# Optimization experiments

Hardware: AMD Instinct MI355X
Metric: run time of the kernel (lower is better)

Reference implementation:

```python
import jax, jax.numpy as jnp
import numpy as np

B, T, C = 512, 256, 384
HEAD = 64

def setup_inputs() -> dict:
    key = jax.random.key(0)
    k1, k2, k3, k4 = jax.random.split(key, 4)
    x = jax.random.normal(k1, (B, T, C), dtype=jnp.float32)
    Wq = jax.random.normal(k2, (C, HEAD), dtype=jnp.float32) * (C ** -0.5)
    Wk = jax.random.normal(k3, (C, HEAD), dtype=jnp.float32) * (C ** -0.5)
    Wv = jax.random.normal(k4, (C, HEAD), dtype=jnp.float32) * (C ** -0.5)
    return {"x": x, "Wq": Wq, "Wk": Wk, "Wv": Wv}

def reference(x, Wq, Wk, Wv):
    # projections (Linear with bias=False): x @ W
    q = jnp.einsum('btc,ch->bth', x, Wq)   # [B,T,H]
    k = jnp.einsum('btc,ch->bth', x, Wk)   # [B,T,H]
    v = jnp.einsum('btc,ch->bth', x, Wv)   # [B,T,H]
    Cdim = x.shape[-1]
    # NOTE: original scales by C**-0.5 where C = nEmbd (not headSize)
    scores = jnp.einsum('bth,bsh->bts', q, k) * (Cdim ** -0.5)  # [B,T,T]
    Tlen = x.shape[1]
    causal = jnp.tril(jnp.ones((Tlen, Tlen), dtype=bool))
    scores = jnp.where(causal, scores, -jnp.inf)
    wei = jax.nn.softmax(scores, axis=-1)
    # dropout omitted (eval mode / deterministic reference)
    out = jnp.einsum('bts,bsh->bth', wei, v)  # [B,T,H]
    return out
```

## Files before the change

kernel.cpp:

```cpp
#include <hip/hip_runtime.h>

#define B_ 512
#define T_ 256
#define C_ 384
#define H_ 64
#define WT_STRIDE (H_ * C_)

typedef __bf16 bf16;
typedef bf16  bf16x8 __attribute__((ext_vector_type(8)));
typedef float f32x4  __attribute__((ext_vector_type(4)));

__global__ void prep_wt(const float* __restrict__ Wq,
                        const float* __restrict__ Wk,
                        const float* __restrict__ Wv,
                        bf16* __restrict__ wt)
{
    int idx = blockIdx.x * 256 + threadIdx.x;
    if (idx >= 3 * WT_STRIDE) return;
    int mat = idx / WT_STRIDE;
    int r   = idx % WT_STRIDE;
    int h   = r / C_;
    int k   = r % C_;
    const float* W = (mat == 0) ? Wq : (mat == 1) ? Wk : Wv;
    wt[idx] = (bf16)W[k * H_ + h];
}

__device__ __forceinline__ bf16x8 cvt8(float4 a, float4 b)
{
    bf16x8 r;
    r[0] = (bf16)a.x; r[1] = (bf16)a.y; r[2] = (bf16)a.z; r[3] = (bf16)a.w;
    r[4] = (bf16)b.x; r[5] = (bf16)b.y; r[6] = (bf16)b.z; r[7] = (bf16)b.w;
    return r;
}

#define SWZ(row, col) ((col) ^ (((row) & 7) << 3))

__device__ __forceinline__ const bf16x8* wts_frag(const bf16* wt_s, int mc, int kk)
{
    int byte = ((mc * 192 + kk) * 2) ^ ((mc & 7) << 4);
    return reinterpret_cast<const bf16x8*>(reinterpret_cast<const char*>(wt_s) + byte);
}

template<int USE_WT>
__global__ __launch_bounds__(512, 1)
void head_fused5(const float* __restrict__ x,
                 const float* __restrict__ Wq,
                 const float* __restrict__ Wk,
                 const float* __restrict__ Wv,
                 const bf16* __restrict__ wt,
                 float* __restrict__ out)
{
    __shared__ bf16 wt_s[3 * 64 * 192];
    __shared__ bf16 k_s[T_ * 64];
    __shared__ bf16 vT_s[H_ * 256];
    __shared__ bf16 p_s[8 * 16 * 64];

    const int tid  = threadIdx.x;
    const int wave = tid >> 6;
    const int lane = tid & 63;
    const int lr   = lane & 15;
    const int lg   = lane >> 4;

    const int b = blockIdx.x;
    const float* xb = x + (size_t)b * T_ * C_;
    bf16* pw = &p_s[wave * 16 * 64];

    bf16x8 qf[2][2];

    #pragma unroll
    for (int p = 0; p < 2; ++p) {
        const int mt = p ? (15 - wave) : wave;
        f32x4 acc[3][4];
        #pragma unroll
        for (int a = 0; a < 3; ++a)
            #pragma unroll
            for (int nw = 0; nw < 4; ++nw)
                acc[a][nw] = (f32x4){0.f, 0.f, 0.f, 0.f};

        #pragma unroll
        for (int half = 0; half < 2; ++half) {
            __syncthreads();
            if (USE_WT) {
                bf16x8 v[9];
                #pragma unroll
                for (int c = 0; c < 9; ++c) {
                    int f16 = c * 512 + tid;
                    int mc  = f16 / 24;
                    int kkc = f16 % 24;
                    v[c] = *reinterpret_cast<const bf16x8*>(
                        wt + mc * 384 + half * 192 + kkc * 8);
                }
                #pragma unroll
                for (int c = 0; c < 9; ++c) {
                    int f16 = c * 512 + tid;
                    int mc  = f16 / 24;
                    int kkc = f16 % 24;
                    int byte = ((mc * 192 + kkc * 8) * 2) ^ ((mc & 7) << 4);
                    *reinterpret_cast<bf16x8*>(
                        reinterpret_cast<char*>(wt_s) + byte) = v[c];
                }
            } else {
                #pragma unroll
                for (int c = 0; c < 9; ++c) {
                    int f16 = c * 512 + tid;
                    int mc  = f16 / 24;
                    int kkc = f16 % 24;
                    int mat = mc >> 6, col = mc & 63;
                    const float* W = (mat == 0) ? Wq : (mat == 1) ? Wk : Wv;
                    bf16x8 vv;
                    #pragma unroll
                    for (int j = 0; j < 8; ++j)
                        vv[j] = (bf16)W[(half * 192 + kkc * 8 + j) * H_ + col];
                    int byte = ((mc * 192 + kkc * 8) * 2) ^ ((mc & 7) << 4);
                    *reinterpret_cast<bf16x8*>(
                        reinterpret_cast<char*>(wt_s) + byte) = vv;
                }
            }
            __syncthreads();

            const float* xrow = xb + (mt * 16 + lr) * C_ + half * 192 + lg * 8;
            float4 xa[6][2];
            #pragma unroll
            for (int ks = 0; ks < 6; ++ks) {
                xa[ks][0] = *reinterpret_cast<const float4*>(xrow + ks * 32);
                xa[ks][1] = *reinterpret_cast<const float4*>(xrow + ks * 32 + 4);
            }
            #pragma unroll
            for (int ks = 0; ks < 6; ++ks) {
                bf16x8 af = cvt8(xa[ks][0], xa[ks][1]);
                const int kk = ks * 32 + lg * 8;
                #pragma unroll
                for (int nw = 0; nw < 4; ++nw) {
                    const int col = nw * 16 + lr;
                    acc[0][nw] = __builtin_amdgcn_mfma_f32_16x16x32_bf16(
                        af, *wts_frag(wt_s, col, kk), acc[0][nw], 0, 0, 0);
                    acc[1][nw] = __builtin_amdgcn_mfma_f32_16x16x32_bf16(
                        af, *wts_frag(wt_s, 64 + col, kk), acc[1][nw], 0, 0, 0);
                    acc[2][nw] = __builtin_amdgcn_mfma_f32_16x16x32_bf16(
                        af, *wts_frag(wt_s, 128 + col, kk), acc[2][nw], 0, 0, 0);
                }
            }
        }

        #pragma unroll
        for (int nw = 0; nw < 4; ++nw) {
            #pragma unroll
            for (int r = 0; r < 4; ++r) {
                int row = mt * 16 + lg * 4 + r;
                int col = nw * 16 + lr;
                k_s[row * 64 + SWZ(row, col)]   = (bf16)acc[1][nw][r];
                vT_s[col * 256 + SWZ(col, row)] = (bf16)acc[2][nw][r];
            }
        }
        #pragma unroll
        for (int nw = 0; nw < 4; ++nw) {
            #pragma unroll
            for (int r = 0; r < 4; ++r) {
                int row = lg * 4 + r;
                pw[row * 64 + SWZ(row, nw * 16 + lr)] = (bf16)acc[0][nw][r];
            }
        }
        asm volatile("s_waitcnt lgkmcnt(0)" ::: "memory");
        __builtin_amdgcn_sched_barrier(0);
        qf[p][0] = *reinterpret_cast<const bf16x8*>(&pw[lr * 64 + SWZ(lr, lg * 8)]);
        qf[p][1] = *reinterpret_cast<const bf16x8*>(&pw[lr * 64 + SWZ(lr, 32 + lg * 8)]);
    }
    __syncthreads();

    const float scale = 0.051031036307982884f;

    #pragma unroll
    for (int p = 0; p < 2; ++p) {
        const int mt  = p ? (15 - wave) : wave;
        const int nkt = mt + 1;

        float m[4], l[4];
        f32x4 oacc[4];
        #pragma unroll
        for (int r = 0; r < 4; ++r) { m[r] = -1e30f; l[r] = 0.f; }
        #pragma unroll
        for (int n = 0; n < 4; ++n) oacc[n] = (f32x4){0.f, 0.f, 0.f, 0.f};

        #pragma unroll
        for (int h = 0; h < 2; ++h) {
            const int vh = (nkt - h * 8) < 8 ? (nkt - h * 8) : 8;
            if (vh > 0) {
                float s[8][4];
                #pragma unroll
                for (int j = 0; j < 8; ++j) {
                    const int kt = h * 8 + j;
                    if (j < vh) {
                        bf16x8 kf0 = *reinterpret_cast<const bf16x8*>(
                            &k_s[(kt * 16 + lr) * 64 + SWZ(lr, lg * 8)]);
                        bf16x8 kf1 = *reinterpret_cast<const bf16x8*>(
                            &k_s[(kt * 16 + lr) * 64 + SWZ(lr, 32 + lg * 8)]);
                        f32x4 sc = (f32x4){0.f, 0.f, 0.f, 0.f};
                        sc = __builtin_amdgcn_mfma_f32_16x16x32_bf16(qf[p][0], kf0, sc, 0, 0, 0);
                        sc = __builtin_amdgcn_mfma_f32_16x16x32_bf16(qf[p][1], kf1, sc, 0, 0, 0);
                        #pragma unroll
                        for (int r = 0; r < 4; ++r) {
                            float v = sc[r] * scale;
                            if (kt == mt && lr > lg * 4 + r) v = -1e30f;
                            s[j][r] = v;
                        }
                    } else {
                        #pragma unroll
                        for (int r = 0; r < 4; ++r) s[j][r] = -1e30f;
                    }
                }

                float f[4];
                #pragma unroll
                for (int r = 0; r < 4; ++r) {
                    float pm = s[0][r];
                    #pragma unroll
                    for (int j = 1; j < 8; ++j) pm = fmaxf(pm, s[j][r]);
                    pm = fmaxf(pm, __shfl_xor(pm, 1));
                    pm = fmaxf(pm, __shfl_xor(pm, 2));
                    pm = fmaxf(pm, __shfl_xor(pm, 4));
                    pm = fmaxf(pm, __shfl_xor(pm, 8));
                    float nm = fmaxf(m[r], pm);
                    f[r] = __expf(m[r] - nm);
                    m[r] = nm;
                    l[r] *= f[r];
                }
                #pragma unroll
                for (int n = 0; n < 4; ++n)
                    #pragma unroll
                    for (int r = 0; r < 4; ++r)
                        oacc[n][r] *= f[r];

                #pragma unroll
                for (int r = 0; r < 4; ++r) {
                    float t = 0.f;
                    #pragma unroll
                    for (int j = 0; j < 8; ++j) {
                        float e = __expf(s[j][r] - m[r]);
                        s[j][r] = e;
                        t += e;
                    }
                    t += __shfl_xor(t, 1);
                    t += __shfl_xor(t, 2);
                    t += __shfl_xor(t, 4);
                    t += __shfl_xor(t, 8);
                    l[r] += t;
                }

                const int nkk = (vh + 1) >> 1;
                #pragma unroll
                for (int kkl = 0; kkl < 4; ++kkl) {
                    if (kkl < nkk) {
                        const int kk = h * 4 + kkl;
                        #pragma unroll
                        for (int r = 0; r < 4; ++r) {
                            int row = lg * 4 + r;
                            pw[row * 64 + SWZ(row, lr)]      = (bf16)s[2 * kkl][r];
                            pw[row * 64 + SWZ(row, 16 + lr)] = (bf16)s[2 * kkl + 1][r];
                        }
                        asm volatile("s_waitcnt lgkmcnt(0)" ::: "memory");
                        __builtin_amdgcn_sched_barrier(0);
                        bf16x8 pf = *reinterpret_cast<const bf16x8*>(
                            &pw[lr * 64 + SWZ(lr, lg * 8)]);
                        #pragma unroll
                        for (int n = 0; n < 4; ++n) {
                            bf16x8 vf = *reinterpret_cast<const bf16x8*>(
                                &vT_s[(n * 16 + lr) * 256 + SWZ(lr, kk * 32 + lg * 8)]);
                            oacc[n] = __builtin_amdgcn_mfma_f32_16x16x32_bf16(pf, vf, oacc[n], 0, 0, 0);
                        }
                    }
                }
            }
        }

        float rin[4];
        #pragma unroll
        for (int r = 0; r < 4; ++r) rin[r] = 1.0f / l[r];
        float* op = out + ((size_t)b * T_ + mt * 16) * H_;
        #pragma unroll
        for (int n = 0; n < 4; ++n)
            #pragma unroll
            for (int r = 0; r < 4; ++r)
                op[(lg * 4 + r) * H_ + n * 16 + lr] = oacc[n][r] * rin[r];
    }
}

extern "C" void kernel_launch(void* const* d_in, const int* in_sizes, int n_in,
                              void* d_out, int out_size, void* d_ws, size_t ws_size,
                              hipStream_t stream)
{
    (void)in_sizes; (void)n_in; (void)out_size;
    const float* x  = (const float*)d_in[0];
    const float* Wq = (const float*)d_in[1];
    const float* Wk = (const float*)d_in[2];
    const float* Wv = (const float*)d_in[3];
    float* o = (float*)d_out;

    if (ws_size >= (size_t)(3 * WT_STRIDE * sizeof(bf16))) {
        bf16* wt = (bf16*)d_ws;
        prep_wt<<<dim3((3 * WT_STRIDE + 255) / 256), dim3(256), 0, stream>>>(Wq, Wk, Wv, wt);
        head_fused5<1><<<dim3(B_), dim3(512), 0, stream>>>(x, Wq, Wk, Wv, wt, o);
    } else {
        head_fused5<0><<<dim3(B_), dim3(512), 0, stream>>>(x, Wq, Wk, Wv, nullptr, o);
    }
}
```

Baseline: 76.99 us.

## Process both query tiles per weight stage and prefetch all x fragments upfront

The QKV projection loop is restructured so each wave handles both of its row tiles in a single pass over each weight half. Weights are staged into shared memory twice instead of four times, and each weight fragment read from LDS feeds two MFMAs. All x rows for both tiles and both halves are loaded and converted to bf16 before any compute, so global loads are issued early. The cost is much higher register pressure (48 bf16x8 A fragments plus 24 accumulators), which could cause spills at 512 threads per block.

New measurement: 94.50 us. 22.7% more time.

```diff
diff --git a/kernel.cpp b/kernel.cpp
--- a/kernel.cpp
+++ b/kernel.cpp
@@ -43,7 +43,7 @@
 
 template<int USE_WT>
 __global__ __launch_bounds__(512, 1)
-void head_fused5(const float* __restrict__ x,
+void head_fused6(const float* __restrict__ x,
                  const float* __restrict__ Wq,
                  const float* __restrict__ Wk,
                  const float* __restrict__ Wv,
@@ -66,90 +66,102 @@
     bf16* pw = &p_s[wave * 16 * 64];
 
     bf16x8 qf[2][2];
-
-    #pragma unroll
-    for (int p = 0; p < 2; ++p) {
-        const int mt = p ? (15 - wave) : wave;
-        f32x4 acc[3][4];
+    bf16x8 af[2][2][6];
+
+    #pragma unroll
+    for (int half = 0; half < 2; ++half) {
+        #pragma unroll
+        for (int tile = 0; tile < 2; ++tile) {
+            const int mt = tile ? (15 - wave) : wave;
+            const float* xrow = xb + (mt * 16 + lr) * C_ + half * 192 + lg * 8;
+            float4 t0[6], t1[6];
+            #pragma unroll
+            for (int ks = 0; ks < 6; ++ks) {
+                t0[ks] = *reinterpret_cast<const float4*>(xrow + ks * 32);
+                t1[ks] = *reinterpret_cast<const float4*>(xrow + ks * 32 + 4);
+            }
+            #pragma unroll
+            for (int ks = 0; ks < 6; ++ks)
+                af[half][tile][ks] = cvt8(t0[ks], t1[ks]);
+        }
+    }
+
+    f32x4 acc[2][3][4];
+    #pragma unroll
+    for (int tile = 0; tile < 2; ++tile)
         #pragma unroll
         for (int a = 0; a < 3; ++a)
             #pragma unroll
             for (int nw = 0; nw < 4; ++nw)
-                acc[a][nw] = (f32x4){0.f, 0.f, 0.f, 0.f};
-
-        #pragma unroll
-        for (int half = 0; half < 2; ++half) {
-            __syncthreads();
-            if (USE_WT) {
-                bf16x8 v[9];
-                #pragma unroll
-                for (int c = 0; c < 9; ++c) {
-                    int f16 = c * 512 + tid;
-                    int mc  = f16 / 24;
-                    int kkc = f16 % 24;
-                    v[c] = *reinterpret_cast<const bf16x8*>(
-                        wt + mc * 384 + half * 192 + kkc * 8);
-                }
-                #pragma unroll
-                for (int c = 0; c < 9; ++c) {
-                    int f16 = c * 512 + tid;
-                    int mc  = f16 / 24;
-                    int kkc = f16 % 24;
-                    int byte = ((mc * 192 + kkc * 8) * 2) ^ ((mc & 7) << 4);
-                    *reinterpret_cast<bf16x8*>(
-                        reinterpret_cast<char*>(wt_s) + byte) = v[c];
-                }
-            } else {
-                #pragma unroll
-                for (int c = 0; c < 9; ++c) {
-                    int f16 = c * 512 + tid;
-                    int mc  = f16 / 24;
-                    int kkc = f16 % 24;
-                    int mat = mc >> 6, col = mc & 63;
-                    const float* W = (mat == 0) ? Wq : (mat == 1) ? Wk : Wv;
-                    bf16x8 vv;
-                    #pragma unroll
-                    for (int j = 0; j < 8; ++j)
-                        vv[j] = (bf16)W[(half * 192 + kkc * 8 + j) * H_ + col];
-                    int byte = ((mc * 192 + kkc * 8) * 2) ^ ((mc & 7) << 4);
-                    *reinterpret_cast<bf16x8*>(
-                        reinterpret_cast<char*>(wt_s) + byte) = vv;
-                }
-            }
-            __syncthreads();
-
-            const float* xrow = xb + (mt * 16 + lr) * C_ + half * 192 + lg * 8;
-            float4 xa[6][2];
-            #pragma unroll
-            for (int ks = 0; ks < 6; ++ks) {
-                xa[ks][0] = *reinterpret_cast<const float4*>(xrow + ks * 32);
-                xa[ks][1] = *reinterpret_cast<const float4*>(xrow + ks * 32 + 4);
-            }
-            #pragma unroll
-            for (int ks = 0; ks < 6; ++ks) {
-                bf16x8 af = cvt8(xa[ks][0], xa[ks][1]);
-                const int kk = ks * 32 + lg * 8;
+                acc[tile][a][nw] = (f32x4){0.f, 0.f, 0.f, 0.f};
+
+    #pragma unroll
+    for (int half = 0; half < 2; ++half) {
+        if (half) __syncthreads();
+        if (USE_WT) {
+            bf16x8 v[9];
+            #pragma unroll
+            for (int c = 0; c < 9; ++c) {
+                int f16 = c * 512 + tid;
+                int mc  = f16 / 24;
+                int kkc = f16 % 24;
+                v[c] = *reinterpret_cast<const bf16x8*>(
+                    wt + mc * 384 + half * 192 + kkc * 8);
+            }
+            #pragma unroll
+            for (int c = 0; c < 9; ++c) {
+                int f16 = c * 512 + tid;
+                int mc  = f16 / 24;
+                int kkc = f16 % 24;
+                int byte = ((mc * 192 + kkc * 8) * 2) ^ ((mc & 7) << 4);
+                *reinterpret_cast<bf16x8*>(reinterpret_cast<char*>(wt_s) + byte) = v[c];
+            }
+        } else {
+            #pragma unroll
+            for (int c = 0; c < 9; ++c) {
+                int f16 = c * 512 + tid;
+                int mc  = f16 / 24;
+                int kkc = f16 % 24;
+                int mat = mc >> 6, col = mc & 63;
+                const float* W = (mat == 0) ? Wq : (mat == 1) ? Wk : Wv;
+                bf16x8 vv;
+                #pragma unroll
+                for (int j = 0; j < 8; ++j)
+                    vv[j] = (bf16)W[(half * 192 + kkc * 8 + j) * H_ + col];
+                int byte = ((mc * 192 + kkc * 8) * 2) ^ ((mc & 7) << 4);
+                *reinterpret_cast<bf16x8*>(reinterpret_cast<char*>(wt_s) + byte) = vv;
+            }
+        }
+        __syncthreads();
+
+        #pragma unroll
+        for (int ks = 0; ks < 6; ++ks) {
+            const int kk = ks * 32 + lg * 8;
+            #pragma unroll
+            for (int mat = 0; mat < 3; ++mat) {
                 #pragma unroll
                 for (int nw = 0; nw < 4; ++nw) {
-                    const int col = nw * 16 + lr;
-                    acc[0][nw] = __builtin_amdgcn_mfma_f32_16x16x32_bf16(
-                        af, *wts_frag(wt_s, col, kk), acc[0][nw], 0, 0, 0);
-                    acc[1][nw] = __builtin_amdgcn_mfma_f32_16x16x32_bf16(
-                        af, *wts_frag(wt_s, 64 + col, kk), acc[1][nw], 0, 0, 0);
-                    acc[2][nw] = __builtin_amdgcn_mfma_f32_16x16x32_bf16(
-                        af, *wts_frag(wt_s, 128 + col, kk), acc[2][nw], 0, 0, 0);
-                }
-            }
-        }
-
+                    bf16x8 bfr = *wts_frag(wt_s, mat * 64 + nw * 16 + lr, kk);
+                    acc[0][mat][nw] = __builtin_amdgcn_mfma_f32_16x16x32_bf16(
+                        af[half][0][ks], bfr, acc[0][mat][nw], 0, 0, 0);
+                    acc[1][mat][nw] = __builtin_amdgcn_mfma_f32_16x16x32_bf16(
+                        af[half][1][ks], bfr, acc[1][mat][nw], 0, 0, 0);
+                }
+            }
+        }
+    }
+
+    #pragma unroll
+    for (int tile = 0; tile < 2; ++tile) {
+        const int mt = tile ? (15 - wave) : wave;
         #pragma unroll
         for (int nw = 0; nw < 4; ++nw) {
             #pragma unroll
             for (int r = 0; r < 4; ++r) {
                 int row = mt * 16 + lg * 4 + r;
                 int col = nw * 16 + lr;
-                k_s[row * 64 + SWZ(row, col)]   = (bf16)acc[1][nw][r];
-                vT_s[col * 256 + SWZ(col, row)] = (bf16)acc[2][nw][r];
+                k_s[row * 64 + SWZ(row, col)]   = (bf16)acc[tile][1][nw][r];
+                vT_s[col * 256 + SWZ(col, row)] = (bf16)acc[tile][2][nw][r];
             }
         }
         #pragma unroll
@@ -157,13 +169,15 @@
             #pragma unroll
             for (int r = 0; r < 4; ++r) {
                 int row = lg * 4 + r;
-                pw[row * 64 + SWZ(row, nw * 16 + lr)] = (bf16)acc[0][nw][r];
+                pw[row * 64 + SWZ(row, nw * 16 + lr)] = (bf16)acc[tile][0][nw][r];
             }
         }
         asm volatile("s_waitcnt lgkmcnt(0)" ::: "memory");
         __builtin_amdgcn_sched_barrier(0);
-        qf[p][0] = *reinterpret_cast<const bf16x8*>(&pw[lr * 64 + SWZ(lr, lg * 8)]);
-        qf[p][1] = *reinterpret_cast<const bf16x8*>(&pw[lr * 64 + SWZ(lr, 32 + lg * 8)]);
+        qf[tile][0] = *reinterpret_cast<const bf16x8*>(&pw[lr * 64 + SWZ(lr, lg * 8)]);
+        qf[tile][1] = *reinterpret_cast<const bf16x8*>(&pw[lr * 64 + SWZ(lr, 32 + lg * 8)]);
+        asm volatile("s_waitcnt lgkmcnt(0)" ::: "memory");
+        __builtin_amdgcn_sched_barrier(0);
     }
     __syncthreads();
 
@@ -298,8 +312,8 @@
     if (ws_size >= (size_t)(3 * WT_STRIDE * sizeof(bf16))) {
         bf16* wt = (bf16*)d_ws;
         prep_wt<<<dim3((3 * WT_STRIDE + 255) / 256), dim3(256), 0, stream>>>(Wq, Wk, Wv, wt);
-        head_fused5<1><<<dim3(B_), dim3(512), 0, stream>>>(x, Wq, Wk, Wv, wt, o);
+        head_fused6<1><<<dim3(B_), dim3(512), 0, stream>>>(x, Wq, Wk, Wv, wt, o);
     } else {
-        head_fused5<0><<<dim3(B_), dim3(512), 0, stream>>>(x, Wq, Wk, Wv, nullptr, o);
-    }
-}
+        head_fused6<0><<<dim3(B_), dim3(512), 0, stream>>>(x, Wq, Wk, Wv, nullptr, o);
+    }
+}
```
